# Kernel tuning notes

Measured on AMD Instinct MI355X. Metric: run time of the kernel, lower is better.

## Reference

```python
import jax, jax.numpy as jnp
import numpy as np

D_MODEL = 1024
N_HEADS = 16
HEAD_DIM = D_MODEL // N_HEADS
BATCH = 2
SEQ = 2048


def setup_inputs() -> dict:
    key = jax.random.key(0)
    ks = jax.random.split(key, 9)
    s = 1.0 / np.sqrt(D_MODEL)
    x = jax.random.normal(ks[0], (BATCH, SEQ, D_MODEL), dtype=jnp.float32)
    # causal mask, broadcastable to (B, H, S, S); positions with 0 are masked out
    mask = jnp.tril(jnp.ones((SEQ, SEQ), dtype=bool))[None, None, :, :]
    Wq = jax.random.normal(ks[1], (D_MODEL, D_MODEL), dtype=jnp.float32) * s
    Wk = jax.random.normal(ks[2], (D_MODEL, D_MODEL), dtype=jnp.float32) * s
    Wv = jax.random.normal(ks[3], (D_MODEL, D_MODEL), dtype=jnp.float32) * s
    Wo = jax.random.normal(ks[4], (D_MODEL, D_MODEL), dtype=jnp.float32) * s
    bq = jnp.zeros((D_MODEL,), jnp.float32)
    bk = jnp.zeros((D_MODEL,), jnp.float32)
    bv = jnp.zeros((D_MODEL,), jnp.float32)
    bo = jnp.zeros((D_MODEL,), jnp.float32)
    return {"x": x, "mask": mask, "Wq": Wq, "bq": bq, "Wk": Wk, "bk": bk,
            "Wv": Wv, "bv": bv, "Wo": Wo, "bo": bo}


def reference(x, mask, Wq, bq, Wk, bk, Wv, bv, Wo, bo):
    B, S, _ = x.shape
    scale = HEAD_DIM ** -0.5
    # nn.Linear: y = x @ W.T + b ; W stored as (out, in)
    def proj(W, b):
        y = jnp.einsum('bsd,ed->bse', x, W) + b
        return y.reshape(B, S, N_HEADS, HEAD_DIM).transpose(0, 2, 1, 3)  # (B,H,S,Dh)
    q = proj(Wq, bq)
    k = proj(Wk, bk)
    v = proj(Wv, bv)
    scores = jnp.einsum('bhqd,bhkd->bhqk', q, k) * scale  # (B,H,S,S)
    scores = jnp.where(mask, scores, jnp.float32(-jnp.inf))
    weights = jax.nn.softmax(scores, axis=-1)
    attn = jnp.einsum('bhqk,bhkd->bhqd', weights, v)
    attn = attn.transpose(0, 2, 1, 3).reshape(B, S, D_MODEL)
    out = jnp.einsum('bsd,ed->bse', attn, Wo) + bo
    return out
```

## Files before the change

kernel.cpp:

```cpp
#include <hip/hip_runtime.h>
#include <hip/hip_bf16.h>

using bf16x8 = __attribute__((ext_vector_type(8))) short;
using f32x4  = __attribute__((ext_vector_type(4))) float;

#define SEQ      2048
#define DMODEL   1024
#define NHEADS   16
#define HDIM     64
#define MROWS    4096

__device__ __forceinline__ unsigned short f2bf(float f) {
  union { float f; unsigned u; } c; c.f = f;
  unsigned r = c.u + 0x7FFFu + ((c.u >> 16) & 1u);
  return (unsigned short)(r >> 16);
}

__device__ __forceinline__ unsigned cvtpk(float a, float b) {
  unsigned r;
  asm("v_cvt_pk_bf16_f32 %0, %1, %2" : "=v"(r) : "v"(a), "v"(b));
  return r;
}

__device__ __forceinline__ void gload16(const void* g, void* s) {
  __builtin_amdgcn_global_load_lds(
      (const __attribute__((address_space(1))) void*)g,
      (__attribute__((address_space(3))) void*)s, 16, 0, 0);
}

__global__ void cvt_all(const float* __restrict__ x,  const float* __restrict__ wq,
                        const float* __restrict__ wk, const float* __restrict__ wv,
                        const float* __restrict__ wo,
                        unsigned short* __restrict__ xb,  unsigned short* __restrict__ wqb,
                        unsigned short* __restrict__ wkb, unsigned short* __restrict__ wvb,
                        unsigned short* __restrict__ wob)
{
  int i = blockIdx.x * blockDim.x + threadIdx.x;
  const float* src; unsigned short* dst; int off;
  if (i < 1048576) { src = x; dst = xb; off = i; }
  else {
    int k = i - 1048576, seg = k >> 18; off = k & 262143;
    if      (seg == 0) { src = wq; dst = wqb; }
    else if (seg == 1) { src = wk; dst = wkb; }
    else if (seg == 2) { src = wv; dst = wvb; }
    else               { src = wo; dst = wob; }
  }
  const float4 v = ((const float4*)src)[off];
  ushort4 o;
  o.x = f2bf(v.x); o.y = f2bf(v.y); o.z = f2bf(v.z); o.w = f2bf(v.w);
  ((ushort4*)dst)[off] = o;
}

__global__ __launch_bounds__(256, 4)
void gemm_qkv(const unsigned short* __restrict__ Ab,
              const unsigned short* __restrict__ Wqb,
              const unsigned short* __restrict__ Wkb,
              const unsigned short* __restrict__ Wvb,
              const float* __restrict__ bq, const float* __restrict__ bk,
              const float* __restrict__ bv,
              unsigned short* __restrict__ Qo, unsigned short* __restrict__ Ko,
              unsigned short* __restrict__ Vto)
{
  __shared__ unsigned short As[128 * 64];
  __shared__ unsigned short Bs[128 * 64];
  const int t  = threadIdx.x;
  const int w  = t >> 6, l = t & 63;
  const int lr = l & 15, lg = l >> 4;
  const int bm = blockIdx.x / 24;
  const int bn = blockIdx.x % 24;
  const int which = bn >> 3;
  const unsigned short* Bsrc = which == 0 ? Wqb : (which == 1 ? Wkb : Wvb);
  const float* biasp = which == 0 ? bq : (which == 1 ? bk : bv);
  const int bnw = bn & 7;
  const int wm = w >> 1, wn = w & 1;

  const char* Agp = (const char*)Ab + (size_t)bm * 128 * 2048;
  const char* Bgp = (const char*)Bsrc + (size_t)bnw * 128 * 2048;

  f32x4 acc[4][4];
  #pragma unroll
  for (int a = 0; a < 4; ++a)
    #pragma unroll
    for (int b = 0; b < 4; ++b) acc[a][b] = (f32x4){0.f, 0.f, 0.f, 0.f};

  for (int kt = 0; kt < 16; ++kt) {
    const int kbyte = kt * 128;
    #pragma unroll
    for (int i = 0; i < 4; ++i) {
      int idx  = i * 256 + t;
      int row  = idx >> 3;
      int colb = (idx & 7) << 4;
      gload16(Agp + (size_t)row * 2048 + kbyte + colb, (char*)As + idx * 16);
      gload16(Bgp + (size_t)row * 2048 + kbyte + colb, (char*)Bs + idx * 16);
    }
    __syncthreads();
    #pragma unroll
    for (int kk = 0; kk < 2; ++kk) {
      bf16x8 af[4], bfr[4];
      #pragma unroll
      for (int x = 0; x < 4; ++x) {
        af[x]  = *(const bf16x8*)&As[(wm * 64 + x * 16 + lr) * 64 + kk * 32 + lg * 8];
        bfr[x] = *(const bf16x8*)&Bs[(wn * 64 + x * 16 + lr) * 64 + kk * 32 + lg * 8];
      }
      #pragma unroll
      for (int xa = 0; xa < 4; ++xa)
        #pragma unroll
        for (int xb = 0; xb < 4; ++xb)
          acc[xa][xb] = __builtin_amdgcn_mfma_f32_16x16x32_bf16(af[xa], bfr[xb], acc[xa][xb], 0, 0, 0);
    }
    __syncthreads();
  }

  #pragma unroll
  for (int xb = 0; xb < 4; ++xb) {
    int colg = bnw * 128 + wn * 64 + xb * 16 + lr;
    int h  = colg >> 6, dh = colg & 63;
    float biasv = biasp[colg];
    #pragma unroll
    for (int xa = 0; xa < 4; ++xa) {
      int row0 = bm * 128 + wm * 64 + xa * 16 + lg * 4;
      #pragma unroll
      for (int i = 0; i < 4; ++i) {
        int m = row0 + i;
        int b = m >> 11, s = m & 2047;
        float v = acc[xa][xb][i] + biasv;
        if (which == 0) {
          Qo[(((size_t)(b * NHEADS + h)) * SEQ + s) * HDIM + dh] = f2bf(v * 0.180336881f);
        } else if (which == 1) {
          Ko[(((size_t)(b * NHEADS + h)) * SEQ + s) * HDIM + dh] = f2bf(v);
        } else {
          Vto[(((size_t)(b * NHEADS + h)) * HDIM + dh) * SEQ + s] = f2bf(v);
        }
      }
    }
  }
}

__device__ __forceinline__ void stage_kv64(const char* Kg, const char* Vg,
                                           char* Kl, char* Vl, int nb, int t)
{
  #pragma unroll
  for (int i = 0; i < 2; ++i) {
    int idx = i * 256 + t;
    int row = idx >> 3, colb = (idx & 7) << 4;
    int scol = colb ^ ((row & 7) << 4);
    gload16(Kg + (size_t)(nb + row) * 128 + scol, Kl + idx * 16);
    gload16(Vg + (size_t)row * 4096 + (size_t)nb * 2 + scol, Vl + idx * 16);
  }
}

__device__ __forceinline__ void attn_sub16(const char* Kl, const char* Vl, char* Pw,
                                           const bf16x8 (&qf)[2], const bf16x8 ones,
                                           f32x4 (&o)[4], f32x4 &accL,
                                           int q0w, int kbase, bool diag, int lr, int lg)
{
  bf16x8 kf[4][2];
  #pragma unroll
  for (int n = 0; n < 4; ++n)
    #pragma unroll
    for (int kk = 0; kk < 2; ++kk)
      kf[n][kk] = *(const bf16x8*)(Kl + (size_t)(n * 16 + lr) * 128 +
                                   ((kk * 64 + lg * 16) ^ ((lr & 7) << 4)));
  f32x4 st[4];
  __builtin_amdgcn_s_setprio(1);
  #pragma unroll
  for (int n = 0; n < 4; ++n) {
    f32x4 acc = (f32x4){0.f, 0.f, 0.f, 0.f};
    #pragma unroll
    for (int kk = 0; kk < 2; ++kk)
      acc = __builtin_amdgcn_mfma_f32_16x16x32_bf16(kf[n][kk], qf[kk], acc, 0, 0, 0);
    st[n] = acc;
  }
  __builtin_amdgcn_s_setprio(0);
  if (diag) {
    #pragma unroll
    for (int n = 0; n < 4; ++n) {
      #pragma unroll
      for (int i = 0; i < 4; ++i) {
        int key = kbase + n * 16 + lg * 4 + i;
        if (key > q0w + lr) st[n][i] = -3.0e38f;
      }
    }
  }
  #pragma unroll
  for (int n = 0; n < 4; ++n) {
    float p0 = exp2f(st[n][0]);
    float p1 = exp2f(st[n][1]);
    float p2 = exp2f(st[n][2]);
    float p3 = exp2f(st[n][3]);
    uint2 pw;
    pw.x = cvtpk(p0, p1);
    pw.y = cvtpk(p2, p3);
    *(uint2*)(Pw + lr * 128 + ((n * 32 + lg * 8) ^ ((lr & 7) << 4))) = pw;
  }
  __builtin_amdgcn_s_setprio(1);
  #pragma unroll
  for (int kk = 0; kk < 2; ++kk) {
    bf16x8 af = *(const bf16x8*)(Pw + lr * 128 + ((kk * 64 + lg * 16) ^ ((lr & 7) << 4)));
    accL = __builtin_amdgcn_mfma_f32_16x16x32_bf16(af, ones, accL, 0, 0, 0);
    #pragma unroll
    for (int n = 0; n < 4; ++n) {
      bf16x8 vf = *(const bf16x8*)(Vl + (size_t)(n * 16 + lr) * 128 +
                    ((kk * 64 + lg * 16) ^ ((lr & 7) << 4)));
      o[n] = __builtin_amdgcn_mfma_f32_16x16x32_bf16(af, vf, o[n], 0, 0, 0);
    }
  }
  __builtin_amdgcn_s_setprio(0);
}

__global__ __launch_bounds__(256, 4)
void attn_fwd(const unsigned short* __restrict__ Q,
              const unsigned short* __restrict__ K,
              const unsigned short* __restrict__ Vt,
              unsigned short* __restrict__ O)
{
  const int t = threadIdx.x;
  const int w = t >> 6, l = t & 63;
  const int lr = l & 15, lg = l >> 4;
  const int bh   = blockIdx.x & 31;
  const int slot = blockIdx.x >> 5;
  const int qt   = (slot < 8)  ? slot
                 : (slot < 16) ? (23 - slot)
                 : (slot < 24) ? slot
                 :               (55 - slot);
  const int b = bh >> 4, h = bh & 15;
  const int q0w = qt * 64 + w * 16;

  const unsigned short* Qp = Q + (size_t)bh * SEQ * HDIM;
  const char* Kg = (const char*)(K  + (size_t)bh * SEQ * HDIM);
  const char* Vg = (const char*)(Vt + (size_t)bh * HDIM * SEQ);

  __shared__ unsigned short Klds[2][64 * 64];
  __shared__ unsigned short Vlds[2][64 * 64];
  __shared__ unsigned short Plds[4][16][64];
  char* Pw = (char*)Plds[w];

  bf16x8 qf[2];
  #pragma unroll
  for (int kk = 0; kk < 2; ++kk)
    qf[kk] = *(const bf16x8*)(Qp + (size_t)(q0w + lr) * HDIM + kk * 32 + lg * 8);

  bf16x8 ones;
  #pragma unroll
  for (int e = 0; e < 8; ++e) ones[e] = (short)0x3F80;

  f32x4 o[4];
  f32x4 accL = (f32x4){0.f, 0.f, 0.f, 0.f};
  #pragma unroll
  for (int n = 0; n < 4; ++n) o[n] = (f32x4){0.f, 0.f, 0.f, 0.f};

  const int trips = qt + 1;

  stage_kv64(Kg, Vg, (char*)Klds[0], (char*)Vlds[0], 0, t);
  if (trips > 1)
    stage_kv64(Kg, Vg, (char*)Klds[1], (char*)Vlds[1], 64, t);

  int cur = 0;
  for (int kb = 0; kb < trips; ++kb) {
    if (kb + 1 < trips)
      asm volatile("s_waitcnt vmcnt(4)" ::: "memory");
    else
      asm volatile("s_waitcnt vmcnt(0)" ::: "memory");
    __builtin_amdgcn_s_barrier();
    asm volatile("" ::: "memory");
    attn_sub16((const char*)Klds[cur], (const char*)Vlds[cur], Pw, qf, ones,
               o, accL, q0w, kb * 64, kb == trips - 1, lr, lg);
    asm volatile("" ::: "memory");
    __builtin_amdgcn_s_barrier();
    asm volatile("" ::: "memory");
    if (kb + 2 < trips)
      stage_kv64(Kg, Vg, (char*)Klds[cur], (char*)Vlds[cur], (kb + 2) * 64, t);
    cur ^= 1;
  }

  #pragma unroll
  for (int n = 0; n < 4; ++n) {
    int col = h * HDIM + n * 16 + lr;
    #pragma unroll
    for (int i = 0; i < 4; ++i) {
      int srow = q0w + lg * 4 + i;
      O[((size_t)(b * SEQ + srow)) * DMODEL + col] = f2bf(o[n][i] / accL[i]);
    }
  }
}

__global__ __launch_bounds__(256, 2)
void gemm_out(const unsigned short* __restrict__ Ab, const unsigned short* __restrict__ Bb,
              const float* __restrict__ bias, float* __restrict__ C)
{
  __shared__ unsigned short As[128 * 64];
  __shared__ unsigned short Bs[64 * 64];
  const int t  = threadIdx.x;
  const int w  = t >> 6, l = t & 63;
  const int lr = l & 15, lg = l >> 4;
  const int bm = blockIdx.x >> 4;
  const int bn = blockIdx.x & 15;
  const int wm = w >> 1, wn = w & 1;

  const char* Agp = (const char*)Ab + (size_t)bm * 128 * 2048;
  const char* Bgp = (const char*)Bb + (size_t)bn * 64 * 2048;

  f32x4 acc[4][2];
  #pragma unroll
  for (int a = 0; a < 4; ++a)
    #pragma unroll
    for (int b = 0; b < 2; ++b) acc[a][b] = (f32x4){0.f, 0.f, 0.f, 0.f};

  for (int kt = 0; kt < 16; ++kt) {
    const int kbyte = kt * 128;
    #pragma unroll
    for (int i = 0; i < 4; ++i) {
      int idx  = i * 256 + t;
      int row  = idx >> 3;
      int colb = (idx & 7) << 4;
      gload16(Agp + (size_t)row * 2048 + kbyte + colb, (char*)As + idx * 16);
    }
    #pragma unroll
    for (int i = 0; i < 2; ++i) {
      int idx  = i * 256 + t;
      int row  = idx >> 3;
      int colb = (idx & 7) << 4;
      gload16(Bgp + (size_t)row * 2048 + kbyte + colb, (char*)Bs + idx * 16);
    }
    __syncthreads();
    #pragma unroll
    for (int kk = 0; kk < 2; ++kk) {
      bf16x8 af[4], bfr[2];
      #pragma unroll
      for (int x = 0; x < 4; ++x)
        af[x]  = *(const bf16x8*)&As[(wm * 64 + x * 16 + lr) * 64 + kk * 32 + lg * 8];
      #pragma unroll
      for (int x = 0; x < 2; ++x)
        bfr[x] = *(const bf16x8*)&Bs[(wn * 32 + x * 16 + lr) * 64 + kk * 32 + lg * 8];
      #pragma unroll
      for (int xa = 0; xa < 4; ++xa)
        #pragma unroll
        for (int xb = 0; xb < 2; ++xb)
          acc[xa][xb] = __builtin_amdgcn_mfma_f32_16x16x32_bf16(af[xa], bfr[xb], acc[xa][xb], 0, 0, 0);
    }
    __syncthreads();
  }
  #pragma unroll
  for (int xb = 0; xb < 2; ++xb) {
    int col = bn * 64 + wn * 32 + xb * 16 + lr;
    float bvv = bias[col];
    #pragma unroll
    for (int xa = 0; xa < 4; ++xa) {
      int row0 = bm * 128 + wm * 64 + xa * 16 + lg * 4;
      #pragma unroll
      for (int i = 0; i < 4; ++i)
        C[(size_t)(row0 + i) * DMODEL + col] = acc[xa][xb][i] + bvv;
    }
  }
}

extern "C" void kernel_launch(void* const* d_in, const int* in_sizes, int n_in,
                              void* d_out, int out_size, void* d_ws, size_t ws_size,
                              hipStream_t stream)
{
  const float* x  = (const float*)d_in[0];
  const float* Wq = (const float*)d_in[2];
  const float* bq = (const float*)d_in[3];
  const float* Wk = (const float*)d_in[4];
  const float* bk = (const float*)d_in[5];
  const float* Wv = (const float*)d_in[6];
  const float* bv = (const float*)d_in[7];
  const float* Wo = (const float*)d_in[8];
  const float* bo = (const float*)d_in[9];

  char* ws = (char*)d_ws;
  const size_t MB = 1024 * 1024;
  unsigned short* xb   = (unsigned short*)(ws + 0);
  unsigned short* Wqb  = (unsigned short*)(ws + 8  * MB);
  unsigned short* Wkb  = (unsigned short*)(ws + 10 * MB);
  unsigned short* Wvb  = (unsigned short*)(ws + 12 * MB);
  unsigned short* Wob  = (unsigned short*)(ws + 14 * MB);
  unsigned short* Qb   = (unsigned short*)(ws + 16 * MB);
  unsigned short* Kb   = (unsigned short*)(ws + 24 * MB);
  unsigned short* Vtb  = (unsigned short*)(ws + 32 * MB);
  unsigned short* Attn = (unsigned short*)(ws + 40 * MB);

  cvt_all<<<8192, 256, 0, stream>>>(x, Wq, Wk, Wv, Wo, xb, Wqb, Wkb, Wvb, Wob);
  gemm_qkv<<<768, 256, 0, stream>>>(xb, Wqb, Wkb, Wvb, bq, bk, bv, Qb, Kb, Vtb);
  attn_fwd<<<1024, 256, 0, stream>>>(Qb, Kb, Vtb, Attn);
  gemm_out<<<512, 256, 0, stream>>>(Attn, Wob, bo, (float*)d_out);
}
```

Baseline: 114.1 us.

## Process 32 query rows per wave in attention, halving block size

Each wave of the attention kernel now handles two 16-row query fragments, so every K and V fragment read from LDS feeds twice as many MFMAs. Blocks shrink from 4 to 2 waves, each thread issues twice as many K/V staging loads, and the wait count is adjusted to match. The exp2f call is replaced with raw v_exp_f32. In exchange, per-thread register pressure roughly doubles for accumulators and there are fewer waves per block to hide load latency.

```diff
diff --git a/kernel.cpp b/kernel.cpp
--- a/kernel.cpp
+++ b/kernel.cpp
@@ -19,6 +19,12 @@
 __device__ __forceinline__ unsigned cvtpk(float a, float b) {
   unsigned r;
   asm("v_cvt_pk_bf16_f32 %0, %1, %2" : "=v"(r) : "v"(a), "v"(b));
+  return r;
+}
+
+__device__ __forceinline__ float fexp2(float x) {
+  float r;
+  asm("v_exp_f32 %0, %1" : "=v"(r) : "v"(x));
   return r;
 }
 
@@ -140,8 +146,8 @@
                                            char* Kl, char* Vl, int nb, int t)
 {
   #pragma unroll
-  for (int i = 0; i < 2; ++i) {
-    int idx = i * 256 + t;
+  for (int i = 0; i < 4; ++i) {
+    int idx = i * 128 + t;
     int row = idx >> 3, colb = (idx & 7) << 4;
     int scol = colb ^ ((row & 7) << 4);
     gload16(Kg + (size_t)(nb + row) * 128 + scol, Kl + idx * 16);
@@ -149,9 +155,9 @@
   }
 }
 
-__device__ __forceinline__ void attn_sub16(const char* Kl, const char* Vl, char* Pw,
-                                           const bf16x8 (&qf)[2], const bf16x8 ones,
-                                           f32x4 (&o)[4], f32x4 &accL,
+__device__ __forceinline__ void attn_sub32(const char* Kl, const char* Vl, char* Pw,
+                                           const bf16x8 (&qf)[2][2], const bf16x8 ones,
+                                           f32x4 (&o)[2][4], f32x4 (&accL)[2],
                                            int q0w, int kbase, bool diag, int lr, int lg)
 {
   bf16x8 kf[4][2];
@@ -161,54 +167,62 @@
     for (int kk = 0; kk < 2; ++kk)
       kf[n][kk] = *(const bf16x8*)(Kl + (size_t)(n * 16 + lr) * 128 +
                                    ((kk * 64 + lg * 16) ^ ((lr & 7) << 4)));
-  f32x4 st[4];
+  f32x4 st[2][4];
   __builtin_amdgcn_s_setprio(1);
   #pragma unroll
-  for (int n = 0; n < 4; ++n) {
-    f32x4 acc = (f32x4){0.f, 0.f, 0.f, 0.f};
-    #pragma unroll
-    for (int kk = 0; kk < 2; ++kk)
-      acc = __builtin_amdgcn_mfma_f32_16x16x32_bf16(kf[n][kk], qf[kk], acc, 0, 0, 0);
-    st[n] = acc;
-  }
+  for (int f = 0; f < 2; ++f)
+    #pragma unroll
+    for (int n = 0; n < 4; ++n) {
+      f32x4 acc = (f32x4){0.f, 0.f, 0.f, 0.f};
+      #pragma unroll
+      for (int kk = 0; kk < 2; ++kk)
+        acc = __builtin_amdgcn_mfma_f32_16x16x32_bf16(kf[n][kk], qf[f][kk], acc, 0, 0, 0);
+      st[f][n] = acc;
+    }
   __builtin_amdgcn_s_setprio(0);
   if (diag) {
     #pragma unroll
+    for (int f = 0; f < 2; ++f)
+      #pragma unroll
+      for (int n = 0; n < 4; ++n)
+        #pragma unroll
+        for (int i = 0; i < 4; ++i) {
+          int key = kbase + n * 16 + lg * 4 + i;
+          if (key > q0w + f * 16 + lr) st[f][n][i] = -3.0e38f;
+        }
+  }
+  #pragma unroll
+  for (int f = 0; f < 2; ++f)
+    #pragma unroll
     for (int n = 0; n < 4; ++n) {
-      #pragma unroll
-      for (int i = 0; i < 4; ++i) {
-        int key = kbase + n * 16 + lg * 4 + i;
-        if (key > q0w + lr) st[n][i] = -3.0e38f;
-      }
-    }
-  }
-  #pragma unroll
-  for (int n = 0; n < 4; ++n) {
-    float p0 = exp2f(st[n][0]);
-    float p1 = exp2f(st[n][1]);
-    float p2 = exp2f(st[n][2]);
-    float p3 = exp2f(st[n][3]);
-    uint2 pw;
-    pw.x = cvtpk(p0, p1);
-    pw.y = cvtpk(p2, p3);
-    *(uint2*)(Pw + lr * 128 + ((n * 32 + lg * 8) ^ ((lr & 7) << 4))) = pw;
-  }
+      float p0 = fexp2(st[f][n][0]);
+      float p1 = fexp2(st[f][n][1]);
+      float p2 = fexp2(st[f][n][2]);
+      float p3 = fexp2(st[f][n][3]);
+      uint2 pw;
+      pw.x = cvtpk(p0, p1);
+      pw.y = cvtpk(p2, p3);
+      *(uint2*)(Pw + f * 2048 + lr * 128 + ((n * 32 + lg * 8) ^ ((lr & 7) << 4))) = pw;
+    }
   __builtin_amdgcn_s_setprio(1);
   #pragma unroll
   for (int kk = 0; kk < 2; ++kk) {
-    bf16x8 af = *(const bf16x8*)(Pw + lr * 128 + ((kk * 64 + lg * 16) ^ ((lr & 7) << 4)));
-    accL = __builtin_amdgcn_mfma_f32_16x16x32_bf16(af, ones, accL, 0, 0, 0);
+    bf16x8 af0 = *(const bf16x8*)(Pw +        lr * 128 + ((kk * 64 + lg * 16) ^ ((lr & 7) << 4)));
+    bf16x8 af1 = *(const bf16x8*)(Pw + 2048 + lr * 128 + ((kk * 64 + lg * 16) ^ ((lr & 7) << 4)));
+    accL[0] = __builtin_amdgcn_mfma_f32_16x16x32_bf16(af0, ones, accL[0], 0, 0, 0);
+    accL[1] = __builtin_amdgcn_mfma_f32_16x16x32_bf16(af1, ones, accL[1], 0, 0, 0);
     #pragma unroll
     for (int n = 0; n < 4; ++n) {
       bf16x8 vf = *(const bf16x8*)(Vl + (size_t)(n * 16 + lr) * 128 +
                     ((kk * 64 + lg * 16) ^ ((lr & 7) << 4)));
-      o[n] = __builtin_amdgcn_mfma_f32_16x16x32_bf16(af, vf, o[n], 0, 0, 0);
+      o[0][n] = __builtin_amdgcn_mfma_f32_16x16x32_bf16(af0, vf, o[0][n], 0, 0, 0);
+      o[1][n] = __builtin_amdgcn_mfma_f32_16x16x32_bf16(af1, vf, o[1][n], 0, 0, 0);
     }
   }
   __builtin_amdgcn_s_setprio(0);
 }
 
-__global__ __launch_bounds__(256, 4)
+__global__ __launch_bounds__(128, 2)
 void attn_fwd(const unsigned short* __restrict__ Q,
               const unsigned short* __restrict__ K,
               const unsigned short* __restrict__ Vt,
@@ -224,7 +238,7 @@
                  : (slot < 24) ? slot
                  :               (55 - slot);
   const int b = bh >> 4, h = bh & 15;
-  const int q0w = qt * 64 + w * 16;
+  const int q0w = qt * 64 + w * 32;
 
   const unsigned short* Qp = Q + (size_t)bh * SEQ * HDIM;
   const char* Kg = (const char*)(K  + (size_t)bh * SEQ * HDIM);
@@ -232,22 +246,28 @@
 
   __shared__ unsigned short Klds[2][64 * 64];
   __shared__ unsigned short Vlds[2][64 * 64];
-  __shared__ unsigned short Plds[4][16][64];
+  __shared__ unsigned short Plds[2][2][16][64];
   char* Pw = (char*)Plds[w];
 
-  bf16x8 qf[2];
-  #pragma unroll
-  for (int kk = 0; kk < 2; ++kk)
-    qf[kk] = *(const bf16x8*)(Qp + (size_t)(q0w + lr) * HDIM + kk * 32 + lg * 8);
+  bf16x8 qf[2][2];
+  #pragma unroll
+  for (int f = 0; f < 2; ++f)
+    #pragma unroll
+    for (int kk = 0; kk < 2; ++kk)
+      qf[f][kk] = *(const bf16x8*)(Qp + (size_t)(q0w + f * 16 + lr) * HDIM + kk * 32 + lg * 8);
 
   bf16x8 ones;
   #pragma unroll
   for (int e = 0; e < 8; ++e) ones[e] = (short)0x3F80;
 
-  f32x4 o[4];
-  f32x4 accL = (f32x4){0.f, 0.f, 0.f, 0.f};
-  #pragma unroll
-  for (int n = 0; n < 4; ++n) o[n] = (f32x4){0.f, 0.f, 0.f, 0.f};
+  f32x4 o[2][4];
+  f32x4 accL[2];
+  #pragma unroll
+  for (int f = 0; f < 2; ++f) {
+    accL[f] = (f32x4){0.f, 0.f, 0.f, 0.f};
+    #pragma unroll
+    for (int n = 0; n < 4; ++n) o[f][n] = (f32x4){0.f, 0.f, 0.f, 0.f};
+  }
 
   const int trips = qt + 1;
 
@@ -258,12 +278,12 @@
   int cur = 0;
   for (int kb = 0; kb < trips; ++kb) {
     if (kb + 1 < trips)
-      asm volatile("s_waitcnt vmcnt(4)" ::: "memory");
+      asm volatile("s_waitcnt vmcnt(8)" ::: "memory");
     else
       asm volatile("s_waitcnt vmcnt(0)" ::: "memory");
     __builtin_amdgcn_s_barrier();
     asm volatile("" ::: "memory");
-    attn_sub16((const char*)Klds[cur], (const char*)Vlds[cur], Pw, qf, ones,
+    attn_sub32((const char*)Klds[cur], (const char*)Vlds[cur], Pw, qf, ones,
                o, accL, q0w, kb * 64, kb == trips - 1, lr, lg);
     asm volatile("" ::: "memory");
     __builtin_amdgcn_s_barrier();
@@ -274,14 +294,16 @@
   }
 
   #pragma unroll
-  for (int n = 0; n < 4; ++n) {
-    int col = h * HDIM + n * 16 + lr;
-    #pragma unroll
-    for (int i = 0; i < 4; ++i) {
-      int srow = q0w + lg * 4 + i;
-      O[((size_t)(b * SEQ + srow)) * DMODEL + col] = f2bf(o[n][i] / accL[i]);
-    }
-  }
+  for (int f = 0; f < 2; ++f)
+    #pragma unroll
+    for (int n = 0; n < 4; ++n) {
+      int col = h * HDIM + n * 16 + lr;
+      #pragma unroll
+      for (int i = 0; i < 4; ++i) {
+        int srow = q0w + f * 16 + lg * 4 + i;
+        O[((size_t)(b * SEQ + srow)) * DMODEL + col] = f2bf(o[f][n][i] / accL[f][i]);
+      }
+    }
 }
 
 __global__ __launch_bounds__(256, 2)
@@ -382,6 +404,6 @@
 
   cvt_all<<<8192, 256, 0, stream>>>(x, Wq, Wk, Wv, Wo, xb, Wqb, Wkb, Wvb, Wob);
   gemm_qkv<<<768, 256, 0, stream>>>(xb, Wqb, Wkb, Wvb, bq, bk, bv, Qb, Kb, Vtb);
-  attn_fwd<<<1024, 256, 0, stream>>>(Qb, Kb, Vtb, Attn);
+  attn_fwd<<<1024, 128, 0, stream>>>(Qb, Kb, Vtb, Attn);
   gemm_out<<<512, 256, 0, stream>>>(Attn, Wob, bo, (float*)d_out);
 }
```

Result: no change. 114.1 us (+0.0%).
